# Kernel tuning notes

Hardware: AMD Instinct MI355X
Metric: run time of the kernel (lower is better)

Reference implementation:

```python
import jax, jax.numpy as jnp
import numpy as np

B, S, E, H = 4, 2048, 1024, 16
D = E // H
N_INF = -10000.0


def setup_inputs() -> dict:
    key = jax.random.key(0)
    ks = jax.random.split(key, 12)
    sc = 1.0 / np.sqrt(E)
    inp = {
        "q": jax.random.normal(ks[0], (B, S, E), jnp.float32),
        "k": jax.random.normal(ks[1], (B, S, E), jnp.float32),
        "v": jax.random.normal(ks[2], (B, S, E), jnp.float32),
        "mask": jax.random.randint(ks[3], (1, 1, S, S), 0, 2, jnp.int32),
        "wq": jax.random.normal(ks[4], (E, E), jnp.float32) * sc,
        "bq": jax.random.normal(ks[5], (E,), jnp.float32) * sc,
        "wk": jax.random.normal(ks[6], (E, E), jnp.float32) * sc,
        "bk": jax.random.normal(ks[7], (E,), jnp.float32) * sc,
        "wv": jax.random.normal(ks[8], (E, E), jnp.float32) * sc,
        "bv": jax.random.normal(ks[9], (E,), jnp.float32) * sc,
        "wo": jax.random.normal(ks[10], (E, E), jnp.float32) * sc,
        "bo": jax.random.normal(ks[11], (E,), jnp.float32) * sc,
    }
    return inp


def _split(x):
    # [B,S,E] -> [B,H,S,D]
    return x.reshape(B, S, H, D).transpose(0, 2, 1, 3)


def reference(q, k, v, mask, wq, bq, wk, bk, wv, bv, wo, bo):
    # Linear projections (torch Linear: x @ W^T + b)
    qh = _split(q @ wq.T + bq)
    kh = _split(k @ wk.T + bk)
    vh = _split(v @ wv.T + bv)
    # scaled dot-product attention
    scores = jnp.einsum("bhqd,bhkd->bhqk", qh, kh) / jnp.sqrt(jnp.float32(D))
    scores = jnp.where(mask == 0, jnp.float32(N_INF), scores)
    attn = jax.nn.softmax(scores, axis=-1)
    out = jnp.einsum("bhqk,bhkd->bhqd", attn, vh)
    # concat heads: [B,H,S,D] -> [B,S,E]
    out = out.transpose(0, 2, 1, 3).reshape(B, S, E)
    return out @ wo.T + bo
```

## Files before the change

kernel.cpp:

```cpp
#include <hip/hip_runtime.h>

typedef __attribute__((ext_vector_type(8))) short short8;
typedef __attribute__((ext_vector_type(4))) short s16x4;
typedef __attribute__((ext_vector_type(4))) float f32x4;
typedef __attribute__((ext_vector_type(4))) int int4v;
typedef __attribute__((ext_vector_type(2))) unsigned int uint2v;
typedef __attribute__((ext_vector_type(4))) unsigned int uint4v;

#define MFMA16x16x32(a, b, c) __builtin_amdgcn_mfma_f32_16x16x32_bf16((a), (b), (c), 0, 0, 0)

#define QK_SCALE 0.18033688011112042f

__device__ __forceinline__ unsigned short f2bf(float f) {
  unsigned u = __builtin_bit_cast(unsigned, f);
  u += 0x7fffu + ((u >> 16) & 1u);
  return (unsigned short)(u >> 16);
}

__device__ __forceinline__ unsigned cvt_pk(float lo, float hi) {
  unsigned r;
  asm("v_cvt_pk_bf16_f32 %0, %1, %2" : "=v"(r) : "v"(lo), "v"(hi));
  return r;
}

__device__ __forceinline__ f32x4 mfma16(s16x4 a, s16x4 b, f32x4 c) {
  f32x4 d;
  asm("v_mfma_f32_16x16x16_bf16 %0, %1, %2, %3" : "=v"(d) : "v"(a), "v"(b), "v"(c));
  return d;
}

__global__ __launch_bounds__(256) void prep_bf16(const float* __restrict__ in,
                                                 unsigned short* __restrict__ out) {
  const int i = (blockIdx.x * 256 + threadIdx.x) * 8;
  f32x4 a = *(const f32x4*)(in + i);
  f32x4 b = *(const f32x4*)(in + i + 4);
  uint4v r;
  r[0] = cvt_pk(a[0], a[1]);
  r[1] = cvt_pk(a[2], a[3]);
  r[2] = cvt_pk(b[0], b[1]);
  r[3] = cvt_pk(b[2], b[3]);
  *(uint4v*)(out + i) = r;
}

__global__ __launch_bounds__(256) void prep_biasf(const int* __restrict__ mask,
                                                  float* __restrict__ bias) {
  const int i = (blockIdx.x * 256 + threadIdx.x) * 8;
  int4v m0 = *(const int4v*)(mask + i);
  int4v m1 = *(const int4v*)(mask + i + 4);
  f32x4 o0, o1;
#pragma unroll
  for (int j = 0; j < 4; ++j) o0[j] = (m0[j] == 0) ? -96.0f : 0.0f;
#pragma unroll
  for (int j = 0; j < 4; ++j) o1[j] = (m1[j] == 0) ? -96.0f : 0.0f;
  *(f32x4*)(bias + i) = o0;
  *(f32x4*)(bias + i + 4) = o1;
}

template <int EPI>
__global__ __launch_bounds__(256) void gemm_bt(
    const unsigned short* __restrict__ A, const unsigned short* __restrict__ B,
    const float* __restrict__ bias, void* __restrict__ out,
    int M, int N, int K, float scl) {
  __shared__ unsigned short Asm[128][72];
  __shared__ unsigned short Bsm[128][72];
  const int tid = threadIdx.x;
  const int lane = tid & 63;
  const int wid = tid >> 6;
  const int wr = wid >> 1, wc = wid & 1;
  const int mbase = blockIdx.y * 128, nbase = blockIdx.x * 128;
  const int srow = tid >> 3, scol = (tid & 7) << 3;

  f32x4 acc[4][4] = {};

  short8 areg[4], breg[4];
#pragma unroll
  for (int r = 0; r < 4; ++r) {
    areg[r] = *(const short8*)(A + (size_t)(mbase + srow + 32 * r) * K + scol);
    breg[r] = *(const short8*)(B + (size_t)(nbase + srow + 32 * r) * K + scol);
  }

  for (int k0 = 0; k0 < K; k0 += 64) {
#pragma unroll
    for (int r = 0; r < 4; ++r) {
      *(short8*)&Asm[srow + 32 * r][scol] = areg[r];
      *(short8*)&Bsm[srow + 32 * r][scol] = breg[r];
    }
    if (k0 + 64 < K) {
#pragma unroll
      for (int r = 0; r < 4; ++r) {
        areg[r] = *(const short8*)(A + (size_t)(mbase + srow + 32 * r) * K + k0 + 64 + scol);
        breg[r] = *(const short8*)(B + (size_t)(nbase + srow + 32 * r) * K + k0 + 64 + scol);
      }
    }
    __syncthreads();
#pragma unroll
    for (int ks = 0; ks < 2; ++ks) {
      const int kk = ks * 32 + (lane >> 4) * 8;
      short8 af[4], bfv[4];
#pragma unroll
      for (int t = 0; t < 4; ++t) {
        af[t] = *(const short8*)&Asm[wr * 64 + t * 16 + (lane & 15)][kk];
        bfv[t] = *(const short8*)&Bsm[wc * 64 + t * 16 + (lane & 15)][kk];
      }
#pragma unroll
      for (int tm = 0; tm < 4; ++tm)
#pragma unroll
        for (int tn = 0; tn < 4; ++tn)
          acc[tm][tn] = MFMA16x16x32(af[tm], bfv[tn], acc[tm][tn]);
    }
    __syncthreads();
  }

  float bn[4];
  if (EPI == 0 || EPI == 2) {
#pragma unroll
    for (int tn = 0; tn < 4; ++tn)
      bn[tn] = bias[nbase + wc * 64 + tn * 16 + (lane & 15)];
  }
  float bm[4][4];
  if (EPI == 1) {
#pragma unroll
    for (int tm = 0; tm < 4; ++tm)
#pragma unroll
      for (int i = 0; i < 4; ++i)
        bm[tm][i] = bias[mbase + wr * 64 + tm * 16 + (lane >> 4) * 4 + i];
  }
#pragma unroll
  for (int tm = 0; tm < 4; ++tm) {
#pragma unroll
    for (int i = 0; i < 4; ++i) {
      const int m = mbase + wr * 64 + tm * 16 + (lane >> 4) * 4 + i;
#pragma unroll
      for (int tn = 0; tn < 4; ++tn) {
        const int n = nbase + wc * 64 + tn * 16 + (lane & 15);
        const float v = (acc[tm][tn][i] + (EPI == 1 ? bm[tm][i] : bn[tn])) * scl;
        if (EPI == 0) {
          const size_t idx =
              (((size_t)(m >> 11) * 16 + (n >> 6)) * 2048 + (m & 2047)) * 64 + (n & 63);
          ((unsigned short*)out)[idx] = f2bf(v);
        } else if (EPI == 1) {
          const size_t idx =
              (((size_t)(n >> 11) * 16 + (m >> 6)) * 64 + (m & 63)) * 2048 + (n & 2047);
          ((unsigned short*)out)[idx] = f2bf(v);
        } else {
          ((float*)out)[(size_t)m * N + n] = v;
        }
      }
    }
  }
}

__global__ __launch_bounds__(256, 2) void attn_fused(
    const unsigned short* __restrict__ Qh, const unsigned short* __restrict__ Kh,
    const unsigned short* __restrict__ VT, const float* __restrict__ Biasf,
    unsigned short* __restrict__ Ob) {
  __shared__ unsigned short Kl[2][64][72];
  __shared__ unsigned short Vl[2][64][72];
  const int tid = threadIdx.x, lane = tid & 63, w = tid >> 6;
  const int m = lane & 15, g = lane >> 4;
  const int wg = ((blockIdx.x & 7) << 7) + (blockIdx.x >> 3);
  const int qt = wg & 15, bh = wg >> 4;
  const int q0 = qt << 7;
  const unsigned short* Qb = Qh + (size_t)bh * (2048 * 64);
  const unsigned short* Kb = Kh + (size_t)bh * (2048 * 64);
  const unsigned short* Vb = VT + (size_t)bh * (64 * 2048);
  const int srow = tid >> 3, scol = (tid & 7) << 3;

  short8 qf[2][2];
#pragma unroll
  for (int ks = 0; ks < 2; ++ks)
#pragma unroll
    for (int tq = 0; tq < 2; ++tq)
      qf[ks][tq] = *(const short8*)(Qb +
          (size_t)(q0 + w * 32 + tq * 16 + m) * 64 + ks * 32 + g * 8);

  const float* brow[2];
#pragma unroll
  for (int tq = 0; tq < 2; ++tq)
    brow[tq] = Biasf + (size_t)(q0 + w * 32 + tq * 16 + m) * 2048 + g * 4;

  f32x4 acc[2][4] = {};
  float l_run[2] = {0.f, 0.f};

  short8 kreg[2], vreg[2];
  kreg[0] = *(const short8*)(Kb + (size_t)srow * 64 + scol);
  kreg[1] = *(const short8*)(Kb + (size_t)(srow + 32) * 64 + scol);
  vreg[0] = *(const short8*)(Vb + (size_t)srow * 2048 + scol);
  vreg[1] = *(const short8*)(Vb + (size_t)(srow + 32) * 2048 + scol);
  *(short8*)&Kl[0][srow][scol] = kreg[0];
  *(short8*)&Kl[0][srow + 32][scol] = kreg[1];
  *(short8*)&Vl[0][srow][scol] = vreg[0];
  *(short8*)&Vl[0][srow + 32][scol] = vreg[1];
  kreg[0] = *(const short8*)(Kb + (size_t)(64 + srow) * 64 + scol);
  kreg[1] = *(const short8*)(Kb + (size_t)(64 + srow + 32) * 64 + scol);
  vreg[0] = *(const short8*)(Vb + (size_t)srow * 2048 + 64 + scol);
  vreg[1] = *(const short8*)(Vb + (size_t)(srow + 32) * 2048 + 64 + scol);
  __syncthreads();

  for (int kt = 0; kt < 32; ++kt) {
    const int buf = kt & 1;
    const int kv0 = kt << 6;

    f32x4 bini[2][4];
#pragma unroll
    for (int tq = 0; tq < 2; ++tq)
#pragma unroll
      for (int tkv = 0; tkv < 4; ++tkv)
        bini[tq][tkv] = *(const f32x4*)(brow[tq] + kv0 + tkv * 16);

    f32x4 st[4][2] = {};
    __builtin_amdgcn_s_setprio(1);
#pragma unroll
    for (int ks = 0; ks < 2; ++ks) {
      const int kk = ks * 32 + g * 8;
      short8 kf[4];
#pragma unroll
      for (int t = 0; t < 4; ++t) kf[t] = *(const short8*)&Kl[buf][t * 16 + m][kk];
#pragma unroll
      for (int tkv = 0; tkv < 4; ++tkv)
#pragma unroll
        for (int tq = 0; tq < 2; ++tq)
          st[tkv][tq] = MFMA16x16x32(kf[tkv], qf[ks][tq], st[tkv][tq]);
    }
    __builtin_amdgcn_s_setprio(0);

    uint2v pa[2][4];
#pragma unroll
    for (int tq = 0; tq < 2; ++tq) {
      float rsum = l_run[tq];
#pragma unroll
      for (int tkv = 0; tkv < 4; ++tkv) {
        const float x0 = __builtin_amdgcn_exp2f(st[tkv][tq][0] + bini[tq][tkv][0]);
        const float x1 = __builtin_amdgcn_exp2f(st[tkv][tq][1] + bini[tq][tkv][1]);
        const float x2 = __builtin_amdgcn_exp2f(st[tkv][tq][2] + bini[tq][tkv][2]);
        const float x3 = __builtin_amdgcn_exp2f(st[tkv][tq][3] + bini[tq][tkv][3]);
        rsum += (x0 + x1) + (x2 + x3);
        pa[tq][tkv][0] = cvt_pk(x0, x1);
        pa[tq][tkv][1] = cvt_pk(x2, x3);
      }
      l_run[tq] = rsum;
    }

    asm volatile("s_nop 1");
    __builtin_amdgcn_s_setprio(1);
#pragma unroll
    for (int tn = 0; tn < 4; ++tn) {
      s16x4 vf[4];
#pragma unroll
      for (int tkv = 0; tkv < 4; ++tkv)
        vf[tkv] = *(const s16x4*)&Vl[buf][tn * 16 + m][tkv * 16 + g * 4];
#pragma unroll
      for (int tm = 0; tm < 2; ++tm)
#pragma unroll
        for (int tkv = 0; tkv < 4; ++tkv)
          acc[tm][tn] = mfma16(__builtin_bit_cast(s16x4, pa[tm][tkv]), vf[tkv], acc[tm][tn]);
    }
    __builtin_amdgcn_s_setprio(0);

    if (kt < 31) {
      *(short8*)&Kl[buf ^ 1][srow][scol] = kreg[0];
      *(short8*)&Kl[buf ^ 1][srow + 32][scol] = kreg[1];
      *(short8*)&Vl[buf ^ 1][srow][scol] = vreg[0];
      *(short8*)&Vl[buf ^ 1][srow + 32][scol] = vreg[1];
      if (kt < 30) {
        const int kv2 = (kt + 2) << 6;
        kreg[0] = *(const short8*)(Kb + (size_t)(kv2 + srow) * 64 + scol);
        kreg[1] = *(const short8*)(Kb + (size_t)(kv2 + srow + 32) * 64 + scol);
        vreg[0] = *(const short8*)(Vb + (size_t)srow * 2048 + kv2 + scol);
        vreg[1] = *(const short8*)(Vb + (size_t)(srow + 32) * 2048 + kv2 + scol);
      }
    }
    __syncthreads();
  }

  asm volatile("s_nop 7\ns_nop 7");

#pragma unroll
  for (int tm = 0; tm < 2; ++tm) {
    l_run[tm] += __shfl_xor(l_run[tm], 16);
    l_run[tm] += __shfl_xor(l_run[tm], 32);
  }

  const int b = bh >> 4, h = bh & 15;
#pragma unroll
  for (int tm = 0; tm < 2; ++tm) {
#pragma unroll
    for (int i = 0; i < 4; ++i) {
      const float lv = __shfl(l_run[tm], (g << 2) + i);
      const float rl = 1.0f / lv;
      const int q = q0 + w * 32 + tm * 16 + (g << 2) + i;
      unsigned short* orow = Ob + ((size_t)b * 2048 + q) * 1024 + h * 64;
#pragma unroll
      for (int tn = 0; tn < 4; ++tn)
        orow[tn * 16 + m] = f2bf(acc[tm][tn][i] * rl);
    }
  }
}

extern "C" void kernel_launch(void* const* d_in, const int* in_sizes, int n_in,
                              void* d_out, int out_size, void* d_ws, size_t ws_size,
                              hipStream_t stream) {
  const float* q = (const float*)d_in[0];
  const float* k = (const float*)d_in[1];
  const float* v = (const float*)d_in[2];
  const int* mask = (const int*)d_in[3];
  const float* wq = (const float*)d_in[4];
  const float* bq = (const float*)d_in[5];
  const float* wk = (const float*)d_in[6];
  const float* bk = (const float*)d_in[7];
  const float* wv = (const float*)d_in[8];
  const float* bv = (const float*)d_in[9];
  const float* wo = (const float*)d_in[10];
  const float* bo = (const float*)d_in[11];

  char* ws = (char*)d_ws;
  unsigned short* Qh = (unsigned short*)ws;
  unsigned short* Kh = (unsigned short*)(ws + (16u << 20));
  unsigned short* VT = (unsigned short*)(ws + (32u << 20));
  float* Biasf = (float*)(ws + (48u << 20));
  unsigned short* S = (unsigned short*)(ws + (64u << 20));
  unsigned short* Ob = S;
  unsigned short* wqb = Kh;
  unsigned short* wkb = VT;
  unsigned short* wvb = (unsigned short*)Biasf;
  unsigned short* wob = Qh;

  const dim3 blk(256);
  prep_bf16<<<dim3(4096), blk, 0, stream>>>(q, S);
  prep_bf16<<<dim3(512), blk, 0, stream>>>(wq, wqb);
  gemm_bt<0><<<dim3(8, 64), blk, 0, stream>>>(S, wqb, bq, (void*)Qh, 8192, 1024, 1024, QK_SCALE);
  prep_bf16<<<dim3(4096), blk, 0, stream>>>(k, S);
  prep_bf16<<<dim3(512), blk, 0, stream>>>(wk, wkb);
  gemm_bt<0><<<dim3(8, 64), blk, 0, stream>>>(S, wkb, bk, (void*)Kh, 8192, 1024, 1024, 1.0f);
  prep_bf16<<<dim3(4096), blk, 0, stream>>>(v, S);
  prep_bf16<<<dim3(512), blk, 0, stream>>>(wv, wvb);
  gemm_bt<1><<<dim3(64, 8), blk, 0, stream>>>(wvb, S, bv, (void*)VT, 1024, 8192, 1024, 1.0f);
  prep_biasf<<<dim3(2048), blk, 0, stream>>>(mask, Biasf);
  attn_fused<<<dim3(1024), blk, 0, stream>>>(Qh, Kh, VT, Biasf, Ob);
  prep_bf16<<<dim3(512), blk, 0, stream>>>(wo, wob);
  gemm_bt<2><<<dim3(8, 64), blk, 0, stream>>>(Ob, wob, bo, d_out, 8192, 1024, 1024, 1.0f);
}
```

Baseline: 296.7 us.

## Fuse fp32-to-bf16 input conversion into GEMMs, use bf16 mask bias, widen attention blocks

The separate activation conversion kernels for q, k and v are removed, and the projection GEMMs now load fp32 directly and convert to bf16 before staging in shared memory. The mask bias is stored as bf16 instead of fp32, halving the bias traffic read by the attention kernel. The attention kernel goes from 256 to 512 threads per block covering 256 query rows, so each K/V tile loaded into shared memory is shared by twice as many query rows. The GEMMs now read fp32 activations, which doubles their global load bytes and register use, and larger attention blocks may reduce occupancy.

```diff
diff --git a/kernel.cpp b/kernel.cpp
--- a/kernel.cpp
+++ b/kernel.cpp
@@ -6,10 +6,12 @@
 typedef __attribute__((ext_vector_type(4))) int int4v;
 typedef __attribute__((ext_vector_type(2))) unsigned int uint2v;
 typedef __attribute__((ext_vector_type(4))) unsigned int uint4v;
+typedef __attribute__((ext_vector_type(4))) unsigned short u16x4;
 
 #define MFMA16x16x32(a, b, c) __builtin_amdgcn_mfma_f32_16x16x32_bf16((a), (b), (c), 0, 0, 0)
 
 #define QK_SCALE 0.18033688011112042f
+#define MASKB_BF16 ((unsigned short)0xC2C0)
 
 __device__ __forceinline__ unsigned short f2bf(float f) {
   unsigned u = __builtin_bit_cast(unsigned, f);
@@ -17,10 +19,23 @@
   return (unsigned short)(u >> 16);
 }
 
+__device__ __forceinline__ float bf2f(unsigned short s) {
+  return __builtin_bit_cast(float, (unsigned)s << 16);
+}
+
 __device__ __forceinline__ unsigned cvt_pk(float lo, float hi) {
   unsigned r;
   asm("v_cvt_pk_bf16_f32 %0, %1, %2" : "=v"(r) : "v"(lo), "v"(hi));
   return r;
+}
+
+__device__ __forceinline__ short8 cvt8v(f32x4 a, f32x4 b) {
+  uint4v r;
+  r[0] = cvt_pk(a[0], a[1]);
+  r[1] = cvt_pk(a[2], a[3]);
+  r[2] = cvt_pk(b[0], b[1]);
+  r[3] = cvt_pk(b[2], b[3]);
+  return __builtin_bit_cast(short8, r);
 }
 
 __device__ __forceinline__ f32x4 mfma16(s16x4 a, s16x4 b, f32x4 c) {
@@ -34,35 +49,33 @@
   const int i = (blockIdx.x * 256 + threadIdx.x) * 8;
   f32x4 a = *(const f32x4*)(in + i);
   f32x4 b = *(const f32x4*)(in + i + 4);
-  uint4v r;
-  r[0] = cvt_pk(a[0], a[1]);
-  r[1] = cvt_pk(a[2], a[3]);
-  r[2] = cvt_pk(b[0], b[1]);
-  r[3] = cvt_pk(b[2], b[3]);
-  *(uint4v*)(out + i) = r;
-}
-
-__global__ __launch_bounds__(256) void prep_biasf(const int* __restrict__ mask,
-                                                  float* __restrict__ bias) {
+  *(short8*)(out + i) = cvt8v(a, b);
+}
+
+__global__ __launch_bounds__(256) void prep_bias(const int* __restrict__ mask,
+                                                 unsigned short* __restrict__ bias) {
   const int i = (blockIdx.x * 256 + threadIdx.x) * 8;
   int4v m0 = *(const int4v*)(mask + i);
   int4v m1 = *(const int4v*)(mask + i + 4);
-  f32x4 o0, o1;
-#pragma unroll
-  for (int j = 0; j < 4; ++j) o0[j] = (m0[j] == 0) ? -96.0f : 0.0f;
-#pragma unroll
-  for (int j = 0; j < 4; ++j) o1[j] = (m1[j] == 0) ? -96.0f : 0.0f;
-  *(f32x4*)(bias + i) = o0;
-  *(f32x4*)(bias + i + 4) = o1;
-}
-
-template <int EPI>
+  short8 s;
+#pragma unroll
+  for (int j = 0; j < 4; ++j) s[j] = (m0[j] == 0) ? (short)MASKB_BF16 : (short)0;
+#pragma unroll
+  for (int j = 0; j < 4; ++j) s[4 + j] = (m1[j] == 0) ? (short)MASKB_BF16 : (short)0;
+  *(short8*)(bias + i) = s;
+}
+
+template <int EPI, bool CA, bool CB>
 __global__ __launch_bounds__(256) void gemm_bt(
-    const unsigned short* __restrict__ A, const unsigned short* __restrict__ B,
+    const void* __restrict__ Av, const void* __restrict__ Bv,
     const float* __restrict__ bias, void* __restrict__ out,
     int M, int N, int K, float scl) {
   __shared__ unsigned short Asm[128][72];
   __shared__ unsigned short Bsm[128][72];
+  const unsigned short* A16 = (const unsigned short*)Av;
+  const float* A32 = (const float*)Av;
+  const unsigned short* B16 = (const unsigned short*)Bv;
+  const float* B32 = (const float*)Bv;
   const int tid = threadIdx.x;
   const int lane = tid & 63;
   const int wid = tid >> 6;
@@ -73,23 +86,55 @@
   f32x4 acc[4][4] = {};
 
   short8 areg[4], breg[4];
+  f32x4 aregf[4][2], bregf[4][2];
+
 #pragma unroll
   for (int r = 0; r < 4; ++r) {
-    areg[r] = *(const short8*)(A + (size_t)(mbase + srow + 32 * r) * K + scol);
-    breg[r] = *(const short8*)(B + (size_t)(nbase + srow + 32 * r) * K + scol);
+    const size_t aoff = (size_t)(mbase + srow + 32 * r) * K + scol;
+    const size_t boff = (size_t)(nbase + srow + 32 * r) * K + scol;
+    if constexpr (CA) {
+      aregf[r][0] = *(const f32x4*)(A32 + aoff);
+      aregf[r][1] = *(const f32x4*)(A32 + aoff + 4);
+    } else {
+      areg[r] = *(const short8*)(A16 + aoff);
+    }
+    if constexpr (CB) {
+      bregf[r][0] = *(const f32x4*)(B32 + boff);
+      bregf[r][1] = *(const f32x4*)(B32 + boff + 4);
+    } else {
+      breg[r] = *(const short8*)(B16 + boff);
+    }
   }
 
   for (int k0 = 0; k0 < K; k0 += 64) {
 #pragma unroll
     for (int r = 0; r < 4; ++r) {
-      *(short8*)&Asm[srow + 32 * r][scol] = areg[r];
-      *(short8*)&Bsm[srow + 32 * r][scol] = breg[r];
+      if constexpr (CA)
+        *(short8*)&Asm[srow + 32 * r][scol] = cvt8v(aregf[r][0], aregf[r][1]);
+      else
+        *(short8*)&Asm[srow + 32 * r][scol] = areg[r];
+      if constexpr (CB)
+        *(short8*)&Bsm[srow + 32 * r][scol] = cvt8v(bregf[r][0], bregf[r][1]);
+      else
+        *(short8*)&Bsm[srow + 32 * r][scol] = breg[r];
     }
     if (k0 + 64 < K) {
 #pragma unroll
       for (int r = 0; r < 4; ++r) {
-        areg[r] = *(const short8*)(A + (size_t)(mbase + srow + 32 * r) * K + k0 + 64 + scol);
-        breg[r] = *(const short8*)(B + (size_t)(nbase + srow + 32 * r) * K + k0 + 64 + scol);
+        const size_t aoff = (size_t)(mbase + srow + 32 * r) * K + k0 + 64 + scol;
+        const size_t boff = (size_t)(nbase + srow + 32 * r) * K + k0 + 64 + scol;
+        if constexpr (CA) {
+          aregf[r][0] = *(const f32x4*)(A32 + aoff);
+          aregf[r][1] = *(const f32x4*)(A32 + aoff + 4);
+        } else {
+          areg[r] = *(const short8*)(A16 + aoff);
+        }
+        if constexpr (CB) {
+          bregf[r][0] = *(const f32x4*)(B32 + boff);
+          bregf[r][1] = *(const f32x4*)(B32 + boff + 4);
+        } else {
+          breg[r] = *(const short8*)(B16 + boff);
+        }
       }
     }
     __syncthreads();
@@ -150,17 +195,17 @@
   }
 }
 
-__global__ __launch_bounds__(256, 2) void attn_fused(
+__global__ __launch_bounds__(512, 2) void attn_fused(
     const unsigned short* __restrict__ Qh, const unsigned short* __restrict__ Kh,
-    const unsigned short* __restrict__ VT, const float* __restrict__ Biasf,
+    const unsigned short* __restrict__ VT, const unsigned short* __restrict__ Bias16,
     unsigned short* __restrict__ Ob) {
   __shared__ unsigned short Kl[2][64][72];
   __shared__ unsigned short Vl[2][64][72];
   const int tid = threadIdx.x, lane = tid & 63, w = tid >> 6;
   const int m = lane & 15, g = lane >> 4;
-  const int wg = ((blockIdx.x & 7) << 7) + (blockIdx.x >> 3);
-  const int qt = wg & 15, bh = wg >> 4;
-  const int q0 = qt << 7;
+  const int wg = ((blockIdx.x & 7) << 6) | (blockIdx.x >> 3);
+  const int qt = wg & 7, bh = wg >> 3;
+  const int q0 = qt << 8;
   const unsigned short* Qb = Qh + (size_t)bh * (2048 * 64);
   const unsigned short* Kb = Kh + (size_t)bh * (2048 * 64);
   const unsigned short* Vb = VT + (size_t)bh * (64 * 2048);
@@ -174,39 +219,33 @@
       qf[ks][tq] = *(const short8*)(Qb +
           (size_t)(q0 + w * 32 + tq * 16 + m) * 64 + ks * 32 + g * 8);
 
-  const float* brow[2];
+  const unsigned short* brow[2];
 #pragma unroll
   for (int tq = 0; tq < 2; ++tq)
-    brow[tq] = Biasf + (size_t)(q0 + w * 32 + tq * 16 + m) * 2048 + g * 4;
+    brow[tq] = Bias16 + (size_t)(q0 + w * 32 + tq * 16 + m) * 2048 + g * 4;
 
   f32x4 acc[2][4] = {};
   float l_run[2] = {0.f, 0.f};
 
-  short8 kreg[2], vreg[2];
-  kreg[0] = *(const short8*)(Kb + (size_t)srow * 64 + scol);
-  kreg[1] = *(const short8*)(Kb + (size_t)(srow + 32) * 64 + scol);
-  vreg[0] = *(const short8*)(Vb + (size_t)srow * 2048 + scol);
-  vreg[1] = *(const short8*)(Vb + (size_t)(srow + 32) * 2048 + scol);
-  *(short8*)&Kl[0][srow][scol] = kreg[0];
-  *(short8*)&Kl[0][srow + 32][scol] = kreg[1];
-  *(short8*)&Vl[0][srow][scol] = vreg[0];
-  *(short8*)&Vl[0][srow + 32][scol] = vreg[1];
-  kreg[0] = *(const short8*)(Kb + (size_t)(64 + srow) * 64 + scol);
-  kreg[1] = *(const short8*)(Kb + (size_t)(64 + srow + 32) * 64 + scol);
-  vreg[0] = *(const short8*)(Vb + (size_t)srow * 2048 + 64 + scol);
-  vreg[1] = *(const short8*)(Vb + (size_t)(srow + 32) * 2048 + 64 + scol);
+  short8 kreg, vreg;
+  kreg = *(const short8*)(Kb + (size_t)srow * 64 + scol);
+  vreg = *(const short8*)(Vb + (size_t)srow * 2048 + scol);
+  *(short8*)&Kl[0][srow][scol] = kreg;
+  *(short8*)&Vl[0][srow][scol] = vreg;
+  kreg = *(const short8*)(Kb + (size_t)(64 + srow) * 64 + scol);
+  vreg = *(const short8*)(Vb + (size_t)srow * 2048 + 64 + scol);
   __syncthreads();
 
   for (int kt = 0; kt < 32; ++kt) {
     const int buf = kt & 1;
     const int kv0 = kt << 6;
 
-    f32x4 bini[2][4];
+    u16x4 bini[2][4];
 #pragma unroll
     for (int tq = 0; tq < 2; ++tq)
 #pragma unroll
       for (int tkv = 0; tkv < 4; ++tkv)
-        bini[tq][tkv] = *(const f32x4*)(brow[tq] + kv0 + tkv * 16);
+        bini[tq][tkv] = *(const u16x4*)(brow[tq] + kv0 + tkv * 16);
 
     f32x4 st[4][2] = {};
     __builtin_amdgcn_s_setprio(1);
@@ -230,10 +269,10 @@
       float rsum = l_run[tq];
 #pragma unroll
       for (int tkv = 0; tkv < 4; ++tkv) {
-        const float x0 = __builtin_amdgcn_exp2f(st[tkv][tq][0] + bini[tq][tkv][0]);
-        const float x1 = __builtin_amdgcn_exp2f(st[tkv][tq][1] + bini[tq][tkv][1]);
-        const float x2 = __builtin_amdgcn_exp2f(st[tkv][tq][2] + bini[tq][tkv][2]);
-        const float x3 = __builtin_amdgcn_exp2f(st[tkv][tq][3] + bini[tq][tkv][3]);
+        const float x0 = __builtin_amdgcn_exp2f(st[tkv][tq][0] + bf2f(bini[tq][tkv][0]));
+        const float x1 = __builtin_amdgcn_exp2f(st[tkv][tq][1] + bf2f(bini[tq][tkv][1]));
+        const float x2 = __builtin_amdgcn_exp2f(st[tkv][tq][2] + bf2f(bini[tq][tkv][2]));
+        const float x3 = __builtin_amdgcn_exp2f(st[tkv][tq][3] + bf2f(bini[tq][tkv][3]));
         rsum += (x0 + x1) + (x2 + x3);
         pa[tq][tkv][0] = cvt_pk(x0, x1);
         pa[tq][tkv][1] = cvt_pk(x2, x3);
@@ -258,16 +297,12 @@
     __builtin_amdgcn_s_setprio(0);
 
     if (kt < 31) {
-      *(short8*)&Kl[buf ^ 1][srow][scol] = kreg[0];
-      *(short8*)&Kl[buf ^ 1][srow + 32][scol] = kreg[1];
-      *(short8*)&Vl[buf ^ 1][srow][scol] = vreg[0];
-      *(short8*)&Vl[buf ^ 1][srow + 32][scol] = vreg[1];
+      *(short8*)&Kl[buf ^ 1][srow][scol] = kreg;
+      *(short8*)&Vl[buf ^ 1][srow][scol] = vreg;
       if (kt < 30) {
         const int kv2 = (kt + 2) << 6;
-        kreg[0] = *(const short8*)(Kb + (size_t)(kv2 + srow) * 64 + scol);
-        kreg[1] = *(const short8*)(Kb + (size_t)(kv2 + srow + 32) * 64 + scol);
-        vreg[0] = *(const short8*)(Vb + (size_t)srow * 2048 + kv2 + scol);
-        vreg[1] = *(const short8*)(Vb + (size_t)(srow + 32) * 2048 + kv2 + scol);
+        kreg = *(const short8*)(Kb + (size_t)(kv2 + srow) * 64 + scol);
+        vreg = *(const short8*)(Vb + (size_t)srow * 2048 + kv2 + scol);
       }
     }
     __syncthreads();
@@ -317,26 +352,26 @@
   unsigned short* Qh = (unsigned short*)ws;
   unsigned short* Kh = (unsigned short*)(ws + (16u << 20));
   unsigned short* VT = (unsigned short*)(ws + (32u << 20));
-  float* Biasf = (float*)(ws + (48u << 20));
-  unsigned short* S = (unsigned short*)(ws + (64u << 20));
-  unsigned short* Ob = S;
+  unsigned short* Bias16 = (unsigned short*)(ws + (48u << 20));
+  unsigned short* Ob = (unsigned short*)(ws + (64u << 20));
   unsigned short* wqb = Kh;
   unsigned short* wkb = VT;
-  unsigned short* wvb = (unsigned short*)Biasf;
+  unsigned short* wvb = Bias16;
   unsigned short* wob = Qh;
 
   const dim3 blk(256);
-  prep_bf16<<<dim3(4096), blk, 0, stream>>>(q, S);
   prep_bf16<<<dim3(512), blk, 0, stream>>>(wq, wqb);
-  gemm_bt<0><<<dim3(8, 64), blk, 0, stream>>>(S, wqb, bq, (void*)Qh, 8192, 1024, 1024, QK_SCALE);
-  prep_bf16<<<dim3(4096), blk, 0, stream>>>(k, S);
+  gemm_bt<0, true, false><<<dim3(8, 64), blk, 0, stream>>>(
+      q, wqb, bq, (void*)Qh, 8192, 1024, 1024, QK_SCALE);
   prep_bf16<<<dim3(512), blk, 0, stream>>>(wk, wkb);
-  gemm_bt<0><<<dim3(8, 64), blk, 0, stream>>>(S, wkb, bk, (void*)Kh, 8192, 1024, 1024, 1.0f);
-  prep_bf16<<<dim3(4096), blk, 0, stream>>>(v, S);
+  gemm_bt<0, true, false><<<dim3(8, 64), blk, 0, stream>>>(
+      k, wkb, bk, (void*)Kh, 8192, 1024, 1024, 1.0f);
   prep_bf16<<<dim3(512), blk, 0, stream>>>(wv, wvb);
-  gemm_bt<1><<<dim3(64, 8), blk, 0, stream>>>(wvb, S, bv, (void*)VT, 1024, 8192, 1024, 1.0f);
-  prep_biasf<<<dim3(2048), blk, 0, stream>>>(mask, Biasf);
-  attn_fused<<<dim3(1024), blk, 0, stream>>>(Qh, Kh, VT, Biasf, Ob);
+  gemm_bt<1, false, true><<<dim3(64, 8), blk, 0, stream>>>(
+      wvb, v, bv, (void*)VT, 1024, 8192, 1024, 1.0f);
+  prep_bias<<<dim3(2048), blk, 0, stream>>>(mask, Bias16);
+  attn_fused<<<dim3(512), dim3(512), 0, stream>>>(Qh, Kh, VT, Bias16, Ob);
   prep_bf16<<<dim3(512), blk, 0, stream>>>(wo, wob);
-  gemm_bt<2><<<dim3(8, 64), blk, 0, stream>>>(Ob, wob, bo, d_out, 8192, 1024, 1024, 1.0f);
-}
+  gemm_bt<2, false, false><<<dim3(8, 64), blk, 0, stream>>>(
+      Ob, wob, bo, d_out, 8192, 1024, 1024, 1.0f);
+}
```

Result: slower. 324.3 us (+9.3%).
